# Performance work log

Hardware: AMD Instinct MI355X
Metric: run time of the kernel (lower is better)

The kernel has to match this reference:

```python
import jax, jax.numpy as jnp
import numpy as np

S = 1    # support_num
K = 20   # KNN neighbor count for conv layers
B, V = 4, 4096


def _normalize(x, axis):
    n = jnp.linalg.norm(x, axis=axis, keepdims=True)
    return x / jnp.maximum(n, 1e-12)


def _knn(v, k):
    # v: (b, n, 3) -> (b, n, k) indices of k nearest (excluding self)
    sq = jnp.sum(v * v, axis=-1)
    dist = sq[:, :, None] + sq[:, None, :] - 2.0 * jnp.einsum('bic,bjc->bij', v, v)
    return jax.lax.top_k(-dist, k + 1)[1][:, :, 1:]


def _gather(feat, idx):
    # feat (b,n,c), idx (b,n,k) -> (b,n,k,c)
    return feat[jnp.arange(feat.shape[0])[:, None, None], idx]


def _dir_norm(verts, idx):
    nb = _gather(verts, idx)                       # (b,v,k,3)
    return _normalize(nb - verts[:, :, None, :], -1)


def _conv_surface(idx, verts, directions, kernel_num):
    b, v, k = idx.shape
    nd = _dir_norm(verts, idx)
    sd = _normalize(directions, 0)                 # (3, S*kernel_num)
    theta = jax.nn.relu(jnp.einsum('bvkc,cm->bvkm', nd, sd))
    theta = theta.reshape(b, v, k, S, kernel_num)
    return jnp.sum(jnp.max(theta, axis=2), axis=2)  # (b,v,kernel_num)


def _conv_layer(idx, verts, fm, W, bias, directions, out_c):
    b, v, k = idx.shape
    nd = _dir_norm(verts, idx)
    sd = _normalize(directions, 0)                 # (3, S*out_c)
    theta = jax.nn.relu(jnp.einsum('bvkc,cm->bvkm', nd, sd))  # (b,v,k,S*out_c)
    fo = fm @ W + bias                             # (b,v,(S+1)*out_c)
    center = fo[:, :, :out_c]
    support = _gather(fo[:, :, out_c:], idx)       # (b,v,k,S*out_c)
    act = (theta * support).reshape(b, v, k, S, out_c)
    return center + jnp.sum(jnp.max(act, axis=2), axis=2)


def _pool(verts, fm, rate, nn, seed):
    b, v, _ = verts.shape
    idx = _knn(verts, nn)
    pooled = jnp.max(_gather(fm, idx), axis=2)
    sel = jax.random.permutation(jax.random.key(seed), v)[: v // rate]
    return verts[:, sel, :], pooled[:, sel, :]


def _ln(x, g, b):
    m = jnp.mean(x, -1, keepdims=True)
    var = jnp.mean(jnp.square(x - m), -1, keepdims=True)
    return (x - m) / jnp.sqrt(var + 1e-6) * g + b


def _mha(q, kv, Win, bin_, Wout, bout, h):
    E = q.shape[-1]
    hd = E // h
    wq, wk, wv = jnp.split(Win, 3, axis=0)
    bq, bk, bv = jnp.split(bin_, 3)

    def heads(x, w, bb_):
        y = x @ w.T + bb_
        return y.reshape(y.shape[0], y.shape[1], h, hd).transpose(0, 2, 1, 3)

    qh, kh, vh = heads(q, wq, bq), heads(kv, wk, bk), heads(kv, wv, bv)
    a = jax.nn.softmax(jnp.einsum('bhqd,bhkd->bhqk', qh, kh) / jnp.sqrt(jnp.float32(hd)), -1)
    o = jnp.einsum('bhqk,bhkd->bhqd', a, vh).transpose(0, 2, 1, 3).reshape(q.shape)
    return o @ Wout.T + bout


def _conv1x1(x, W, b):
    # x (B,C,N,1) -> (B,O,N,1)
    return jnp.einsum('bcnl,oc->bonl', x, W) + b[None, :, None, None]


def _bn_train(x, g, b):
    # BatchNorm2d in training mode (batch statistics), eps=1e-5
    m = jnp.mean(x, axis=(0, 2, 3), keepdims=True)
    v = jnp.var(x, axis=(0, 2, 3), keepdims=True)
    return (x - m) / jnp.sqrt(v + 1e-5) * g[None, :, None, None] + b[None, :, None, None]


def _forward(vertices, d0, g0, be0, w1, b1, dir1, g1, be1, w2, b2, dir2, g2, be2,
             w3, b3, dir3, g3, be3, token, a1_in_w, a1_in_b, a1_out_w, a1_out_b,
             ffn1_w, ffn1_b, bg, bb, ffn2_w, ffn2_b, a2_in_w, a2_in_b, a2_out_w,
             a2_out_b, w7, b7, dir7, g4, be4, c8_w, c8_b):
    b = vertices.shape[0]
    v0 = vertices[:, 0]                                 # (b, 4096, 3)
    idx0 = _knn(v0, K)
    fm0 = jax.nn.relu(_ln(_conv_surface(idx0, v0, d0, 32), g0, be0))
    fm1 = jax.nn.relu(_ln(_conv_layer(idx0, v0, fm0, w1, b1, dir1, 64), g1, be1))
    v1, fm1 = _pool(v0, fm1, 4, 4, 1)                   # (b,1024,3), (b,1024,64)
    idx1 = _knn(v1, K)
    fm_x = fm1
    fm2 = jax.nn.relu(_ln(_conv_layer(idx1, v1, fm1, w2, b2, dir2, 128), g2, be2))
    fm3 = jax.nn.relu(_ln(_conv_layer(idx1, v1, fm2, w3, b3, dir3, 256), g3, be3))
    _, fm3 = _pool(v1, fm3, 4, 4, 2)                    # (b,256,256)
    tok = jnp.tile(token, (b, 1, 1, 1))[:, :, :, 0].transpose(0, 2, 1)  # (b,1024,64)
    query = _mha(tok, fm_x, a1_in_w, a1_in_b, a1_out_w, a1_out_b, 4) + fm_x
    q2 = query.transpose(0, 2, 1)[:, :, :, None]        # (b,64,1024,1)
    q2 = _conv1x1(jax.nn.relu(_bn_train(_conv1x1(q2, ffn1_w, ffn1_b), bg, bb)), ffn2_w, ffn2_b)
    query = q2[:, :, :, 0].transpose(0, 2, 1)           # (b,1024,256)
    cross = _mha(query, fm3, a2_in_w, a2_in_b, a2_out_w, a2_out_b, 4) + query
    fmf = jax.nn.relu(_ln(_conv_layer(idx1, v1, cross, w7, b7, dir7, 1024), g4, be4))
    fmf = fmf.transpose(0, 2, 1)[:, :, :, None]         # (b,1024,1024,1)
    return _conv1x1(fmf, c8_w, c8_b)                    # (b,256,1024,1)


def setup_inputs():
    ks = iter(jax.random.split(jax.random.key(0), 64))

    def rn(shape, s=0.05):
        return jax.random.normal(next(ks), shape, dtype=jnp.float32) * s

    f32 = jnp.float32
    return dict(
        vertices=jax.random.normal(next(ks), (B, 1, V, 3), dtype=f32),
        d0=rn((3, S * 32)), g0=jnp.ones((32,), f32), be0=jnp.zeros((32,), f32),
        w1=rn((32, (S + 1) * 64)), b1=rn(((S + 1) * 64,)), dir1=rn((3, S * 64)),
        g1=jnp.ones((64,), f32), be1=jnp.zeros((64,), f32),
        w2=rn((64, (S + 1) * 128)), b2=rn(((S + 1) * 128,)), dir2=rn((3, S * 128)),
        g2=jnp.ones((128,), f32), be2=jnp.zeros((128,), f32),
        w3=rn((128, (S + 1) * 256)), b3=rn(((S + 1) * 256,)), dir3=rn((3, S * 256)),
        g3=jnp.ones((256,), f32), be3=jnp.zeros((256,), f32),
        token=rn((1, 64, 1024, 1), 1.0),
        a1_in_w=rn((192, 64)), a1_in_b=rn((192,)), a1_out_w=rn((64, 64)), a1_out_b=rn((64,)),
        ffn1_w=rn((256, 64)), ffn1_b=rn((256,)), bg=jnp.ones((256,), f32), bb=jnp.zeros((256,), f32),
        ffn2_w=rn((256, 256)), ffn2_b=rn((256,)),
        a2_in_w=rn((768, 256)), a2_in_b=rn((768,)), a2_out_w=rn((256, 256)), a2_out_b=rn((256,)),
        w7=rn((256, (S + 1) * 1024)), b7=rn(((S + 1) * 1024,)), dir7=rn((3, S * 1024)),
        g4=jnp.ones((1024,), f32), be4=jnp.zeros((1024,), f32),
        c8_w=rn((256, 1024)), c8_b=rn((256,)),
    )


def reference(vertices, d0, g0, be0, w1, b1, dir1, g1, be1, w2, b2, dir2, g2, be2,
              w3, b3, dir3, g3, be3, token, a1_in_w, a1_in_b, a1_out_w, a1_out_b,
              ffn1_w, ffn1_b, bg, bb, ffn2_w, ffn2_b, a2_in_w, a2_in_b, a2_out_w,
              a2_out_b, w7, b7, dir7, g4, be4, c8_w, c8_b):
    return _forward(vertices, d0, g0, be0, w1, b1, dir1, g1, be1, w2, b2, dir2, g2,
                    be2, w3, b3, dir3, g3, be3, token, a1_in_w, a1_in_b, a1_out_w,
                    a1_out_b, ffn1_w, ffn1_b, bg, bb, ffn2_w, ffn2_b, a2_in_w,
                    a2_in_b, a2_out_w, a2_out_b, w7, b7, dir7, g4, be4, c8_w, c8_b)
```

## Files before the change

kernel.cpp:

```cpp
#include <hip/hip_runtime.h>
#include <stdint.h>
#include <stddef.h>

#define FINF __builtin_inff()

__device__ inline void tf2x32(uint32_t k0, uint32_t k1, uint32_t x0, uint32_t x1,
                              uint32_t* o0, uint32_t* o1) {
  uint32_t ks2 = k0 ^ k1 ^ 0x1BD11BDAu;
  uint32_t v0 = x0 + k0, v1 = x1 + k1;
#define TFR(r) { v0 += v1; v1 = (v1 << (r)) | (v1 >> (32 - (r))); v1 ^= v0; }
  TFR(13) TFR(15) TFR(26) TFR(6)
  v0 += k1;  v1 += ks2 + 1u;
  TFR(17) TFR(29) TFR(16) TFR(24)
  v0 += ks2; v1 += k0 + 2u;
  TFR(13) TFR(15) TFR(26) TFR(6)
  v0 += k0;  v1 += k1 + 3u;
  TFR(17) TFR(29) TFR(16) TFR(24)
  v0 += k1;  v1 += ks2 + 4u;
  TFR(13) TFR(15) TFR(26) TFR(6)
  v0 += ks2; v1 += k0 + 5u;
#undef TFR
  *o0 = v0; *o1 = v1;
}

__global__ __launch_bounds__(1024) void perm_both_kernel(int* __restrict__ sel1,
                                                         int* __restrict__ sel2) {
  __shared__ unsigned long long keys[4096];
  __shared__ int vals[4096];
  __shared__ uint32_t kst[2];
  __shared__ uint32_t sk[2];
  uint32_t seed = (blockIdx.x == 0) ? 1u : 2u;
  int n       = (blockIdx.x == 0) ? 4096 : 1024;
  int rounds  = (blockIdx.x == 0) ? 2 : 1;
  int m       = (blockIdx.x == 0) ? 1024 : 256;
  int* out    = (blockIdx.x == 0) ? sel1 : sel2;
  int t = threadIdx.x;
  for (int i = t; i < n; i += 1024) vals[i] = i;
  if (t == 0) { kst[0] = 0u; kst[1] = seed; }
  __syncthreads();
  for (int r = 0; r < rounds; r++) {
    if (t == 0) {
      uint32_t a0, a1, b0, b1;
      tf2x32(kst[0], kst[1], 0u, 0u, &a0, &a1);
      tf2x32(kst[0], kst[1], 0u, 1u, &b0, &b1);
      kst[0] = a0; kst[1] = a1; sk[0] = b0; sk[1] = b1;
    }
    __syncthreads();
    uint32_t s0 = sk[0], s1 = sk[1];
    for (int i = t; i < n; i += 1024) {
      uint32_t y0, y1; tf2x32(s0, s1, 0u, (uint32_t)i, &y0, &y1);
      keys[i] = ((unsigned long long)(y0 ^ y1) << 32) | (unsigned)i;
    }
    __syncthreads();
    for (int kk = 2; kk <= n; kk <<= 1) {
      for (int j = kk >> 1; j > 0; j >>= 1) {
        for (int i = t; i < n; i += 1024) {
          int l = i ^ j;
          if (l > i) {
            unsigned long long ki = keys[i], kl = keys[l];
            bool up = ((i & kk) == 0);
            if (up ? (ki > kl) : (ki < kl)) {
              keys[i] = kl; keys[l] = ki;
              int v = vals[i]; vals[i] = vals[l]; vals[l] = v;
            }
          }
        }
        __syncthreads();
      }
    }
  }
  for (int i = t; i < m; i += 1024) out[i] = vals[i];
}

__device__ inline void wave_argmin2(float head_d, int head_i, float* Mo, int* wio) {
  float M = head_d;
#pragma unroll
  for (int off = 1; off < 64; off <<= 1) M = fminf(M, __shfl_xor(M, off));
  int cand = (head_d == M) ? head_i : 0x7fffffff;
#pragma unroll
  for (int off = 1; off < 64; off <<= 1) cand = min(cand, __shfl_xor(cand, off));
  *Mo = M; *wio = cand;
}

template <int CNT, int WAVES>
__global__ __launch_bounds__(64 * WAVES) void knn_lex_kernel(const float* __restrict__ verts,
                                                             int N,
                                                             int* __restrict__ idx20,
                                                             int* __restrict__ idx4) {
  int row = blockIdx.x; int b = row / N, i = row - b * N;
  int t = threadIdx.x; int w = t >> 6; int lane = t & 63;
  const float* vb = verts + (size_t)b * N * 3;
  float xi = vb[i * 3], yi = vb[i * 3 + 1], zi = vb[i * 3 + 2];
  float sqi = (xi * xi + yi * yi) + zi * zi;

  int base = w * (N / WAVES) + lane;
  float qd[CNT]; int qi[CNT];
#pragma unroll
  for (int m = 0; m < CNT; m++) {
    int j = base + m * 64;
    float xj = vb[j * 3], yj = vb[j * 3 + 1], zj = vb[j * 3 + 2];
    float sqj = (xj * xj + yj * yj) + zj * zj;
    float dot = (xi * xj + yi * yj) + zi * zj;
    qd[m] = sqi + sqj - 2.f * dot;
    qi[m] = j;
  }
#pragma unroll
  for (int k = 2; k <= CNT; k <<= 1)
#pragma unroll
    for (int j = k >> 1; j > 0; j >>= 1)
#pragma unroll
      for (int m = 0; m < CNT; m++) {
        int l = m ^ j;
        if (l > m) {
          bool up = ((m & k) == 0);
          bool sw = up ? (qd[m] > qd[l]) : (qd[m] < qd[l]);
          float td = sw ? qd[l] : qd[m]; qd[l] = sw ? qd[m] : qd[l]; qd[m] = td;
          int ti = sw ? qi[l] : qi[m]; qi[l] = sw ? qi[m] : qi[l]; qi[m] = ti;
        }
      }

  __shared__ float wd[WAVES][21];
  __shared__ int wi[WAVES][21];
  for (int r = 0; r < 21; r++) {
    float M; int widx;
    wave_argmin2(qd[0], qi[0], &M, &widx);
    if (lane == 0) { wd[w][r] = M; wi[w][r] = widx; }
    bool win = (qi[0] == widx);
#pragma unroll
    for (int m = 0; m < CNT - 1; m++) {
      qd[m] = win ? qd[m + 1] : qd[m];
      qi[m] = win ? qi[m + 1] : qi[m];
    }
    if (win) { qd[CNT - 1] = FINF; qi[CNT - 1] = 0x7fffffff; }
  }
  __syncthreads();
  if (lane < 21) {
    float d0 = wd[w][lane]; int i0 = wi[w][lane];
    int rank = lane;
#pragma unroll
    for (int w2 = 0; w2 < WAVES; w2++) {
      if (w2 == w) continue;
      for (int p = 0; p < 21; p++) {
        float ld = wd[w2][p]; int li = wi[w2][p];
        rank += (ld < d0 || (ld == d0 && li < i0)) ? 1 : 0;
      }
    }
    if (rank >= 1 && rank <= 20) idx20[(size_t)row * 20 + (rank - 1)] = i0;
    if (rank >= 1 && rank <= 4)  idx4[(size_t)row * 4 + (rank - 1)] = i0;
  }
}

template <int CNT>
__global__ __launch_bounds__(64) void knn_1w_lex_kernel(const float* __restrict__ verts, int N,
                                                        int* __restrict__ idx20,
                                                        int* __restrict__ idx4) {
  int row = blockIdx.x; int b = row / N, i = row - b * N;
  int lane = threadIdx.x;
  const float* vb = verts + (size_t)b * N * 3;
  float xi = vb[i * 3], yi = vb[i * 3 + 1], zi = vb[i * 3 + 2];
  float sqi = (xi * xi + yi * yi) + zi * zi;

  float qd[CNT]; int qi[CNT];
#pragma unroll
  for (int m = 0; m < CNT; m++) {
    int j = lane + m * 64;
    float xj = vb[j * 3], yj = vb[j * 3 + 1], zj = vb[j * 3 + 2];
    float sqj = (xj * xj + yj * yj) + zj * zj;
    float dot = (xi * xj + yi * yj) + zi * zj;
    qd[m] = sqi + sqj - 2.f * dot;
    qi[m] = j;
  }
#pragma unroll
  for (int k = 2; k <= CNT; k <<= 1)
#pragma unroll
    for (int j = k >> 1; j > 0; j >>= 1)
#pragma unroll
      for (int m = 0; m < CNT; m++) {
        int l = m ^ j;
        if (l > m) {
          bool up = ((m & k) == 0);
          bool sw = up ? (qd[m] > qd[l]) : (qd[m] < qd[l]);
          float td = sw ? qd[l] : qd[m]; qd[l] = sw ? qd[m] : qd[l]; qd[m] = td;
          int ti = sw ? qi[l] : qi[m]; qi[l] = sw ? qi[m] : qi[l]; qi[m] = ti;
        }
      }
  for (int r = 0; r < 21; r++) {
    float M; int widx;
    wave_argmin2(qd[0], qi[0], &M, &widx);
    if (lane == 0 && r >= 1) {
      idx20[(size_t)row * 20 + (r - 1)] = widx;
      if (r <= 4) idx4[(size_t)row * 4 + (r - 1)] = widx;
    }
    bool win = (qi[0] == widx);
#pragma unroll
    for (int m = 0; m < CNT - 1; m++) {
      qd[m] = win ? qd[m + 1] : qd[m];
      qi[m] = win ? qi[m + 1] : qi[m];
    }
    if (win) { qd[CNT - 1] = FINF; qi[CNT - 1] = 0x7fffffff; }
  }
}

__global__ void conv_surface_kernel(const float* __restrict__ verts,
                                    const int* __restrict__ idx20,
                                    const float* __restrict__ d0,
                                    const float* __restrict__ g, const float* __restrict__ be,
                                    float* __restrict__ out, int N) {
  int row = blockIdx.x; int b = row / N, i = row - b * N;
  int t = threadIdx.x;
  __shared__ float nd[20][3];
  const float* vb = verts + (size_t)b * N * 3;
  if (t < 20) {
    int j = idx20[(size_t)row * 20 + t];
    float dx = vb[j * 3] - vb[i * 3], dy = vb[j * 3 + 1] - vb[i * 3 + 1], dz = vb[j * 3 + 2] - vb[i * 3 + 2];
    float n2 = sqrtf(dx * dx + dy * dy + dz * dz); n2 = fmaxf(n2, 1e-12f);
    nd[t][0] = dx / n2; nd[t][1] = dy / n2; nd[t][2] = dz / n2;
  }
  __syncthreads();
  float x = 0.f;
  if (t < 32) {
    float a = d0[t], bb2 = d0[32 + t], c = d0[64 + t];
    float nrm = fmaxf(sqrtf(a * a + bb2 * bb2 + c * c), 1e-12f);
    a /= nrm; bb2 /= nrm; c /= nrm;
    float mx = -FINF;
    for (int kk = 0; kk < 20; kk++) {
      float th = fmaxf(nd[kk][0] * a + nd[kk][1] * bb2 + nd[kk][2] * c, 0.f);
      mx = fmaxf(mx, th);
    }
    x = mx;
  }
  float s = x;
  for (int off = 32; off; off >>= 1) s += __shfl_xor(s, off);
  float mean = s / 32.f;
  float dev = (t < 32) ? x - mean : 0.f;
  float s2 = dev * dev;
  for (int off = 32; off; off >>= 1) s2 += __shfl_xor(s2, off);
  float var = s2 / 32.f;
  if (t < 32) {
    float y = (x - mean) / sqrtf(var + 1e-6f) * g[t] + be[t];
    out[(size_t)row * 32 + t] = fmaxf(y, 0.f);
  }
}

__global__ void gemm_io_kernel(const float* __restrict__ x, const float* __restrict__ W,
                               const float* __restrict__ bias, float* __restrict__ y,
                               int R, int I, int O) {
  int rb = blockIdx.x * 8;
  int o = blockIdx.y * blockDim.x + threadIdx.x;
  __shared__ float xs[256][8];
  for (int u = 0; u < 8; u++)
    for (int i2 = threadIdx.x; i2 < I; i2 += blockDim.x) xs[i2][u] = x[(size_t)(rb + u) * I + i2];
  __syncthreads();
  float a[8] = {0, 0, 0, 0, 0, 0, 0, 0};
  for (int k2 = 0; k2 < I; k2++) {
    float wv = W[(size_t)k2 * O + o];
    float4 xa = *(const float4*)&xs[k2][0];
    float4 xb = *(const float4*)&xs[k2][4];
    a[0] += xa.x * wv; a[1] += xa.y * wv; a[2] += xa.z * wv; a[3] += xa.w * wv;
    a[4] += xb.x * wv; a[5] += xb.y * wv; a[6] += xb.z * wv; a[7] += xb.w * wv;
  }
  float bv = bias[o];
#pragma unroll
  for (int u = 0; u < 8; u++) y[(size_t)(rb + u) * O + o] = a[u] + bv;
}

template <int CPT>
__global__ void combine_kernel(const float* __restrict__ verts, const int* __restrict__ idx20,
                               const float* __restrict__ fo, const float* __restrict__ dirs,
                               const float* __restrict__ g, const float* __restrict__ be,
                               float* __restrict__ out, int N, int C) {
  int row = blockIdx.x; int b = row / N, i = row - b * N;
  int t = threadIdx.x, bs = blockDim.x;
  __shared__ float nd[20][3];
  __shared__ int nidx[20];
  __shared__ float red[8];
  const float* vb = verts + (size_t)b * N * 3;
  if (t < 20) {
    int j = idx20[(size_t)row * 20 + t];
    nidx[t] = j;
    float dx = vb[j * 3] - vb[i * 3], dy = vb[j * 3 + 1] - vb[i * 3 + 1], dz = vb[j * 3 + 2] - vb[i * 3 + 2];
    float n2 = fmaxf(sqrtf(dx * dx + dy * dy + dz * dz), 1e-12f);
    nd[t][0] = dx / n2; nd[t][1] = dy / n2; nd[t][2] = dz / n2;
  }
  __syncthreads();
  const float* fob = fo + (size_t)b * N * 2 * C;
  const float* forow = fob + (size_t)i * 2 * C;
  float da[CPT], db[CPT], dc[CPT], mx[CPT];
#pragma unroll
  for (int u = 0; u < CPT; u++) {
    int c = t + u * bs;
    float a = dirs[c], bb = dirs[C + c], cc = dirs[2 * C + c];
    float nrm = fmaxf(sqrtf(a * a + bb * bb + cc * cc), 1e-12f);
    da[u] = a / nrm; db[u] = bb / nrm; dc[u] = cc / nrm;
    mx[u] = -FINF;
  }
  for (int kk = 0; kk < 20; kk++) {
    float n0 = nd[kk][0], n1 = nd[kk][1], n2v = nd[kk][2];
    const float* sup = fob + (size_t)nidx[kk] * 2 * C + C + t;
#pragma unroll
    for (int u = 0; u < CPT; u++) {
      float th = fmaxf(n0 * da[u] + n1 * db[u] + n2v * dc[u], 0.f);
      mx[u] = fmaxf(mx[u], th * sup[u * bs]);
    }
  }
  float xv[CPT];
  float ssum = 0.f;
#pragma unroll
  for (int u = 0; u < CPT; u++) {
    int c = t + u * bs;
    float val = forow[c] + mx[u];
    xv[u] = val; ssum += val;
  }
  int nw = bs >> 6;
  for (int off = 32; off; off >>= 1) ssum += __shfl_down(ssum, off);
  if ((t & 63) == 0) red[t >> 6] = ssum;
  __syncthreads();
  if (t == 0) { float s = red[0]; for (int w = 1; w < nw; w++) s += red[w]; red[0] = s; }
  __syncthreads();
  float mean = red[0] / (float)C;
  __syncthreads();
  float s2 = 0.f;
#pragma unroll
  for (int u = 0; u < CPT; u++) { float d2 = xv[u] - mean; s2 += d2 * d2; }
  for (int off = 32; off; off >>= 1) s2 += __shfl_down(s2, off);
  if ((t & 63) == 0) red[t >> 6] = s2;
  __syncthreads();
  if (t == 0) { float s = red[0]; for (int w = 1; w < nw; w++) s += red[w]; red[0] = s; }
  __syncthreads();
  float inv = 1.0f / sqrtf(red[0] / (float)C + 1e-6f);
#pragma unroll
  for (int u = 0; u < CPT; u++) {
    int c = t + u * bs;
    float yv = (xv[u] - mean) * inv * g[c] + be[c];
    out[(size_t)row * C + c] = fmaxf(yv, 0.f);
  }
}

__global__ void pool_select_kernel(const float* __restrict__ fm, const int* __restrict__ idx4,
                                   const int* __restrict__ sel, const float* __restrict__ vin,
                                   float* __restrict__ vout, float* __restrict__ out,
                                   int N, int M, int C) {
  int row = blockIdx.x; int b = row / M, r = row - b * M;
  int s = sel[r];
  const int* id = idx4 + ((size_t)b * N + s) * 4;
  int i0 = id[0], i1 = id[1], i2 = id[2], i3 = id[3];
  const float* fb = fm + (size_t)b * N * C;
  for (int c = threadIdx.x; c < C; c += blockDim.x) {
    float m = fmaxf(fmaxf(fb[(size_t)i0 * C + c], fb[(size_t)i1 * C + c]),
                    fmaxf(fb[(size_t)i2 * C + c], fb[(size_t)i3 * C + c]));
    out[((size_t)b * M + r) * C + c] = m;
  }
  if (vout != nullptr && threadIdx.x < 3)
    vout[((size_t)b * M + r) * 3 + threadIdx.x] = vin[((size_t)b * N + s) * 3 + threadIdx.x];
}

__global__ void tok_kernel(const float* __restrict__ token, float* __restrict__ tok) {
  int id = blockIdx.x * 256 + threadIdx.x;
  int e = id & 63; int n = (id >> 6) & 1023;
  tok[id] = token[e * 1024 + n];
}

__global__ void linear_oi_kernel(const float* __restrict__ x, const float* __restrict__ W,
                                 const float* __restrict__ bias, const float* __restrict__ res,
                                 float* __restrict__ y, int R, int I, int O) {
  int rb = blockIdx.x * 8;
  int o = threadIdx.x;
  __shared__ float xs[8][256];
  for (int u = 0; u < 8; u++)
    for (int i2 = threadIdx.x; i2 < I; i2 += O) xs[u][i2] = x[(size_t)(rb + u) * I + i2];
  __syncthreads();
  float a[8] = {0, 0, 0, 0, 0, 0, 0, 0};
  const float* w = W + (size_t)o * I;
  for (int k2 = 0; k2 < I; k2++) {
    float wv = w[k2];
#pragma unroll
    for (int u = 0; u < 8; u++) a[u] += xs[u][k2] * wv;
  }
  float bv = bias[o];
#pragma unroll
  for (int u = 0; u < 8; u++) {
    float val = a[u] + bv;
    if (res) val += res[(size_t)(rb + u) * O + o];
    y[(size_t)(rb + u) * O + o] = val;
  }
}

template <int HD, int QPT, int KS>
__global__ __launch_bounds__(256) void attn_tiled(
    const float* __restrict__ q, const float* __restrict__ kk,
    const float* __restrict__ vv, float* __restrict__ o,
    int Lq, int Lk, int H, float scale) {
  constexpr int TK = 64;
  constexpr int QG = 256 / (2 * KS);
  constexpr int QPB = QG * QPT;
  constexpr int V4 = HD / 4;
  constexpr int STR = V4 + 1;
  constexpr int HH = HD / 2;
  constexpr int V4H = HH / 4;

  __shared__ float4 Ks[TK * STR];
  __shared__ float4 Vs[TK * STR];

  int t = threadIdx.x;
  int dh = t & 1;
  int ki = (t >> 1) & (KS - 1);
  int qg = t / (2 * KS);
  int nqt = Lq / QPB;
  int qt = blockIdx.x % nqt, bh = blockIdx.x / nqt;
  int h = bh % H, b = bh / H;
  int E = H * HD;
  int q0 = qt * QPB + qg * QPT;

  const float* qbase = q + ((size_t)b * Lq + q0) * E + h * HD + dh * HH;
  const float* kbase = kk + (size_t)b * Lk * E + h * HD;
  const float* vbase = vv + (size_t)b * Lk * E + h * HD;

  float qr[QPT][HH], O[QPT][HH], m[QPT], l[QPT];
#pragma unroll
  for (int r = 0; r < QPT; r++) {
    m[r] = -FINF; l[r] = 0.f;
#pragma unroll
    for (int d = 0; d < HH; d++) { qr[r][d] = qbase[(size_t)r * E + d]; O[r][d] = 0.f; }
  }

  for (int k0 = 0; k0 < Lk; k0 += TK) {
    __syncthreads();
    for (int e = t; e < TK * V4; e += 256) {
      int rr = e / V4, cc = e - rr * V4;
      Ks[rr * STR + cc] = *(const float4*)(kbase + (size_t)(k0 + rr) * E + cc * 4);
      Vs[rr * STR + cc] = *(const float4*)(vbase + (size_t)(k0 + rr) * E + cc * 4);
    }
    __syncthreads();
#pragma unroll 1
    for (int g = 0; g < TK / KS; g += 4) {
      float sc[QPT][4];
#pragma unroll
      for (int jj = 0; jj < 4; jj++) {
        int kl = (g + jj) * KS + ki;
        float sh[QPT];
#pragma unroll
        for (int r = 0; r < QPT; r++) sh[r] = 0.f;
        const float4* kr = &Ks[kl * STR + dh * V4H];
#pragma unroll
        for (int c = 0; c < V4H; c++) {
          float4 kv = kr[c];
#pragma unroll
          for (int r = 0; r < QPT; r++)
            sh[r] += qr[r][4 * c] * kv.x + qr[r][4 * c + 1] * kv.y
                   + qr[r][4 * c + 2] * kv.z + qr[r][4 * c + 3] * kv.w;
        }
#pragma unroll
        for (int r = 0; r < QPT; r++)
          sc[r][jj] = (sh[r] + __shfl_xor(sh[r], 1)) * scale;
      }
#pragma unroll
      for (int r = 0; r < QPT; r++) {
        float tm = fmaxf(fmaxf(sc[r][0], sc[r][1]), fmaxf(sc[r][2], sc[r][3]));
        float nm = fmaxf(m[r], tm);
        float a = __expf(m[r] - nm);
        m[r] = nm;
        float ls = l[r] * a;
#pragma unroll
        for (int d = 0; d < HH; d++) O[r][d] *= a;
#pragma unroll
        for (int jj = 0; jj < 4; jj++) { sc[r][jj] = __expf(sc[r][jj] - nm); ls += sc[r][jj]; }
        l[r] = ls;
      }
#pragma unroll
      for (int jj = 0; jj < 4; jj++) {
        int kl = (g + jj) * KS + ki;
        const float4* vr = &Vs[kl * STR + dh * V4H];
#pragma unroll
        for (int c = 0; c < V4H; c++) {
          float4 v4 = vr[c];
#pragma unroll
          for (int r = 0; r < QPT; r++) {
            O[r][4 * c]     += sc[r][jj] * v4.x;
            O[r][4 * c + 1] += sc[r][jj] * v4.y;
            O[r][4 * c + 2] += sc[r][jj] * v4.z;
            O[r][4 * c + 3] += sc[r][jj] * v4.w;
          }
        }
      }
    }
  }
#pragma unroll
  for (int r = 0; r < QPT; r++) {
    float M = m[r];
#pragma unroll
    for (int mask = 2; mask < 2 * KS; mask <<= 1) M = fmaxf(M, __shfl_xor(M, mask));
    float w = __expf(m[r] - M);
    float ll = l[r] * w;
#pragma unroll
    for (int mask = 2; mask < 2 * KS; mask <<= 1) ll += __shfl_xor(ll, mask);
    float inv = 1.f / ll;
#pragma unroll
    for (int d = 0; d < HH; d++) {
      float x = O[r][d] * w;
#pragma unroll
      for (int mask = 2; mask < 2 * KS; mask <<= 1) x += __shfl_xor(x, mask);
      O[r][d] = x * inv;
    }
  }
  if (ki == 0) {
    float* obase = o + ((size_t)b * Lq + q0) * E + h * HD + dh * HH;
#pragma unroll
    for (int r = 0; r < QPT; r++)
#pragma unroll
      for (int d = 0; d < HH; d++) obase[(size_t)r * E + d] = O[r][d];
  }
}

__global__ void bn_stats_kernel(const float* __restrict__ x, float* __restrict__ stats,
                                int R, int C) {
  int c = blockIdx.x; int t = threadIdx.x;
  __shared__ float red[8];
  float s = 0.f;
  for (int r = t; r < R; r += blockDim.x) s += x[(size_t)r * C + c];
  for (int off = 32; off; off >>= 1) s += __shfl_down(s, off);
  if ((t & 63) == 0) red[t >> 6] = s;
  __syncthreads();
  if (t == 0) { float a = red[0]; for (int w = 1; w < (int)(blockDim.x >> 6); w++) a += red[w]; red[0] = a; }
  __syncthreads();
  float mean = red[0] / (float)R;
  __syncthreads();
  float s2 = 0.f;
  for (int r = t; r < R; r += blockDim.x) { float d = x[(size_t)r * C + c] - mean; s2 += d * d; }
  for (int off = 32; off; off >>= 1) s2 += __shfl_down(s2, off);
  if ((t & 63) == 0) red[t >> 6] = s2;
  __syncthreads();
  if (t == 0) {
    float a = red[0]; for (int w = 1; w < (int)(blockDim.x >> 6); w++) a += red[w];
    stats[c] = mean; stats[C + c] = a / (float)R;
  }
}

__global__ void bn_apply_kernel(float* __restrict__ x, const float* __restrict__ stats,
                                const float* __restrict__ g, const float* __restrict__ b2,
                                int total, int C) {
  int id = blockIdx.x * blockDim.x + threadIdx.x;
  if (id >= total) return;
  int c = id % C;
  float y = (x[id] - stats[c]) / sqrtf(stats[C + c] + 1e-5f) * g[c] + b2[c];
  x[id] = fmaxf(y, 0.f);
}

__global__ void final_kernel(const float* __restrict__ fmf, const float* __restrict__ W,
                             const float* __restrict__ bias, float* __restrict__ out) {
  int nb = blockIdx.x * 8;
  int o = threadIdx.x;
  __shared__ float xs[1024][8];
  for (int u = 0; u < 8; u++)
    for (int c = threadIdx.x; c < 1024; c += 256) xs[c][u] = fmf[(size_t)(nb + u) * 1024 + c];
  __syncthreads();
  float acc[8] = {0, 0, 0, 0, 0, 0, 0, 0};
  const float* w = W + (size_t)o * 1024;
  for (int c = 0; c < 1024; c++) {
    float wv = w[c];
    float4 xa = *(const float4*)&xs[c][0];
    float4 xb = *(const float4*)&xs[c][4];
    acc[0] += xa.x * wv; acc[1] += xa.y * wv; acc[2] += xa.z * wv; acc[3] += xa.w * wv;
    acc[4] += xb.x * wv; acc[5] += xb.y * wv; acc[6] += xb.z * wv; acc[7] += xb.w * wv;
  }
  float bv = bias[o];
#pragma unroll
  for (int u = 0; u < 8; u++) {
    int r = nb + u; int b = r >> 10; int n = r & 1023;
    out[((size_t)(b * 256 + o) << 10) + n] = acc[u] + bv;
  }
}

extern "C" void kernel_launch(void* const* d_in, const int* in_sizes, int n_in,
                              void* d_out, int out_size, void* d_ws, size_t ws_size,
                              hipStream_t stream) {
  (void)in_sizes; (void)n_in; (void)out_size;
  const float* vertices = (const float*)d_in[0];
  const float* d0       = (const float*)d_in[1];
  const float* g0       = (const float*)d_in[2];
  const float* be0      = (const float*)d_in[3];
  const float* w1       = (const float*)d_in[4];
  const float* b1       = (const float*)d_in[5];
  const float* dir1     = (const float*)d_in[6];
  const float* g1       = (const float*)d_in[7];
  const float* be1      = (const float*)d_in[8];
  const float* w2       = (const float*)d_in[9];
  const float* b2       = (const float*)d_in[10];
  const float* dir2     = (const float*)d_in[11];
  const float* g2       = (const float*)d_in[12];
  const float* be2      = (const float*)d_in[13];
  const float* w3       = (const float*)d_in[14];
  const float* b3       = (const float*)d_in[15];
  const float* dir3     = (const float*)d_in[16];
  const float* g3       = (const float*)d_in[17];
  const float* be3      = (const float*)d_in[18];
  const float* token    = (const float*)d_in[19];
  const float* a1_in_w  = (const float*)d_in[20];
  const float* a1_in_b  = (const float*)d_in[21];
  const float* a1_out_w = (const float*)d_in[22];
  const float* a1_out_b = (const float*)d_in[23];
  const float* ffn1_w   = (const float*)d_in[24];
  const float* ffn1_b   = (const float*)d_in[25];
  const float* bg       = (const float*)d_in[26];
  const float* bbp      = (const float*)d_in[27];
  const float* ffn2_w   = (const float*)d_in[28];
  const float* ffn2_b   = (const float*)d_in[29];
  const float* a2_in_w  = (const float*)d_in[30];
  const float* a2_in_b  = (const float*)d_in[31];
  const float* a2_out_w = (const float*)d_in[32];
  const float* a2_out_b = (const float*)d_in[33];
  const float* w7       = (const float*)d_in[34];
  const float* b7       = (const float*)d_in[35];
  const float* dir7     = (const float*)d_in[36];
  const float* g4       = (const float*)d_in[37];
  const float* be4      = (const float*)d_in[38];
  const float* c8_w     = (const float*)d_in[39];
  const float* c8_b     = (const float*)d_in[40];
  float* out = (float*)d_out;
  float* ws = (float*)d_ws;

  if (ws_size < 78568448u) return;

  float* FO     = ws + 0;
  float* S1     = ws + 8388608;
  float* S2     = ws + 12582912;
  float* S3     = ws + 13631488;
  float* QUERY2 = ws + 14680064;
  float* CROSS  = ws + 15728640;
  float* FM1P   = ws + 16777216;
  float* FM3P   = FM1P + 262144;
  float* TOK    = FM3P + 262144;
  float* Q1     = TOK + 262144;
  float* K1     = Q1 + 262144;
  float* VA1    = K1 + 262144;
  float* ATT1   = VA1 + 262144;
  float* K2     = ATT1 + 262144;
  float* V2     = K2 + 262144;
  float* V1     = V2 + 262144;
  float* BNST   = V1 + 12288;
  int* IDX20_0  = (int*)(BNST + 512);
  int* IDX4_0   = IDX20_0 + 327680;
  int* IDX20_1  = IDX4_0 + 65536;
  int* IDX4_1   = IDX20_1 + 81920;
  int* SEL1     = IDX4_1 + 16384;
  int* SEL2     = SEL1 + 1024;

  perm_both_kernel<<<2, 1024, 0, stream>>>(SEL1, SEL2);

  knn_lex_kernel<32, 2><<<4 * 4096, 128, 0, stream>>>(vertices, 4096, IDX20_0, IDX4_0);
  conv_surface_kernel<<<4 * 4096, 64, 0, stream>>>(vertices, IDX20_0, d0, g0, be0, S2, 4096);
  gemm_io_kernel<<<dim3(2048, 1), 128, 0, stream>>>(S2, w1, b1, FO, 16384, 32, 128);
  combine_kernel<1><<<16384, 64, 0, stream>>>(vertices, IDX20_0, FO, dir1, g1, be1, S1, 4096, 64);
  pool_select_kernel<<<4096, 64, 0, stream>>>(S1, IDX4_0, SEL1, vertices, V1, FM1P, 4096, 1024, 64);

  knn_1w_lex_kernel<16><<<4 * 1024, 64, 0, stream>>>(V1, 1024, IDX20_1, IDX4_1);
  gemm_io_kernel<<<dim3(512, 1), 256, 0, stream>>>(FM1P, w2, b2, FO, 4096, 64, 256);
  combine_kernel<1><<<4096, 128, 0, stream>>>(V1, IDX20_1, FO, dir2, g2, be2, S2, 1024, 128);
  gemm_io_kernel<<<dim3(512, 2), 256, 0, stream>>>(S2, w3, b3, FO, 4096, 128, 512);
  combine_kernel<1><<<4096, 256, 0, stream>>>(V1, IDX20_1, FO, dir3, g3, be3, S3, 1024, 256);
  pool_select_kernel<<<1024, 256, 0, stream>>>(S3, IDX4_1, SEL2, nullptr, nullptr, FM3P, 1024, 256, 256);

  tok_kernel<<<1024, 256, 0, stream>>>(token, TOK);
  linear_oi_kernel<<<512, 64, 0, stream>>>(TOK, a1_in_w, a1_in_b, nullptr, Q1, 4096, 64, 64);
  linear_oi_kernel<<<512, 64, 0, stream>>>(FM1P, a1_in_w + 64 * 64, a1_in_b + 64, nullptr, K1, 4096, 64, 64);
  linear_oi_kernel<<<512, 64, 0, stream>>>(FM1P, a1_in_w + 128 * 64, a1_in_b + 128, nullptr, VA1, 4096, 64, 64);
  attn_tiled<16, 4, 8><<<256, 256, 0, stream>>>(Q1, K1, VA1, ATT1, 1024, 1024, 4, 0.25f);
  linear_oi_kernel<<<512, 64, 0, stream>>>(ATT1, a1_out_w, a1_out_b, FM1P, S3, 4096, 64, 64);

  linear_oi_kernel<<<512, 256, 0, stream>>>(S3, ffn1_w, ffn1_b, nullptr, S2, 4096, 64, 256);
  bn_stats_kernel<<<256, 256, 0, stream>>>(S2, BNST, 4096, 256);
  bn_apply_kernel<<<4096, 256, 0, stream>>>(S2, BNST, bg, bbp, 4096 * 256, 256);
  linear_oi_kernel<<<512, 256, 0, stream>>>(S2, ffn2_w, ffn2_b, nullptr, QUERY2, 4096, 256, 256);

  linear_oi_kernel<<<512, 256, 0, stream>>>(QUERY2, a2_in_w, a2_in_b, nullptr, S3, 4096, 256, 256);
  linear_oi_kernel<<<128, 256, 0, stream>>>(FM3P, a2_in_w + 256 * 256, a2_in_b + 256, nullptr, K2, 1024, 256, 256);
  linear_oi_kernel<<<128, 256, 0, stream>>>(FM3P, a2_in_w + 512 * 256, a2_in_b + 512, nullptr, V2, 1024, 256, 256);
  attn_tiled<64, 2, 8><<<512, 256, 0, stream>>>(S3, K2, V2, S1, 1024, 256, 4, 0.125f);
  linear_oi_kernel<<<512, 256, 0, stream>>>(S1, a2_out_w, a2_out_b, QUERY2, CROSS, 4096, 256, 256);

  gemm_io_kernel<<<dim3(512, 8), 256, 0, stream>>>(CROSS, w7, b7, FO, 4096, 256, 2048);
  combine_kernel<4><<<4096, 256, 0, stream>>>(V1, IDX20_1, FO, dir7, g4, be4, S1, 1024, 1024);
  final_kernel<<<512, 256, 0, stream>>>(S1, c8_w, c8_b, out);
}
```

Baseline: 1.006 ms.

## Replace single-block bitonic permutation sort with parallel rank-by-counting kernels

Moves the random-permutation generation off a two-block bitonic sort in shared memory and onto multiple small kernels. One kernel generates threefry sort keys, the other computes each element's rank by counting smaller keys across many blocks, then scatters it. The sequential sort chain on one CU goes away in exchange for six launches and O(n^2) comparisons. Scratch keys live in the IDX20_0 buffer, which is overwritten later by the first KNN kernel.

After: 1.249 ms. +24.1%, slower.

```diff
diff --git a/kernel.cpp b/kernel.cpp
--- a/kernel.cpp
+++ b/kernel.cpp
@@ -23,53 +23,42 @@
   *o0 = v0; *o1 = v1;
 }
 
-__global__ __launch_bounds__(1024) void perm_both_kernel(int* __restrict__ sel1,
-                                                         int* __restrict__ sel2) {
-  __shared__ unsigned long long keys[4096];
-  __shared__ int vals[4096];
-  __shared__ uint32_t kst[2];
-  __shared__ uint32_t sk[2];
-  uint32_t seed = (blockIdx.x == 0) ? 1u : 2u;
-  int n       = (blockIdx.x == 0) ? 4096 : 1024;
-  int rounds  = (blockIdx.x == 0) ? 2 : 1;
-  int m       = (blockIdx.x == 0) ? 1024 : 256;
-  int* out    = (blockIdx.x == 0) ? sel1 : sel2;
+__device__ inline void perm_subkey(uint32_t seed, int round, uint32_t* s0, uint32_t* s1) {
+  uint32_t k0 = 0u, k1 = seed;
+  for (int r = 0; r < round; r++) {
+    uint32_t a0, a1; tf2x32(k0, k1, 0u, 0u, &a0, &a1);
+    k0 = a0; k1 = a1;
+  }
+  tf2x32(k0, k1, 0u, 1u, s0, s1);
+}
+
+__global__ __launch_bounds__(256) void perm_keys_kernel(uint32_t seed, int round, int n,
+                                                        unsigned long long* __restrict__ keys) {
+  uint32_t s0, s1; perm_subkey(seed, round, &s0, &s1);
+  int i = blockIdx.x * 256 + threadIdx.x;
+  if (i < n) {
+    uint32_t y0, y1; tf2x32(s0, s1, 0u, (uint32_t)i, &y0, &y1);
+    keys[i] = ((unsigned long long)(y0 ^ y1) << 32) | (unsigned)i;
+  }
+}
+
+__global__ __launch_bounds__(256) void perm_rank_kernel(const unsigned long long* __restrict__ keys,
+                                                        const int* __restrict__ vin,
+                                                        int* __restrict__ vout, int n, int m) {
+  __shared__ int part[256];
   int t = threadIdx.x;
-  for (int i = t; i < n; i += 1024) vals[i] = i;
-  if (t == 0) { kst[0] = 0u; kst[1] = seed; }
-  __syncthreads();
-  for (int r = 0; r < rounds; r++) {
-    if (t == 0) {
-      uint32_t a0, a1, b0, b1;
-      tf2x32(kst[0], kst[1], 0u, 0u, &a0, &a1);
-      tf2x32(kst[0], kst[1], 0u, 1u, &b0, &b1);
-      kst[0] = a0; kst[1] = a1; sk[0] = b0; sk[1] = b1;
-    }
-    __syncthreads();
-    uint32_t s0 = sk[0], s1 = sk[1];
-    for (int i = t; i < n; i += 1024) {
-      uint32_t y0, y1; tf2x32(s0, s1, 0u, (uint32_t)i, &y0, &y1);
-      keys[i] = ((unsigned long long)(y0 ^ y1) << 32) | (unsigned)i;
-    }
-    __syncthreads();
-    for (int kk = 2; kk <= n; kk <<= 1) {
-      for (int j = kk >> 1; j > 0; j >>= 1) {
-        for (int i = t; i < n; i += 1024) {
-          int l = i ^ j;
-          if (l > i) {
-            unsigned long long ki = keys[i], kl = keys[l];
-            bool up = ((i & kk) == 0);
-            if (up ? (ki > kl) : (ki < kl)) {
-              keys[i] = kl; keys[l] = ki;
-              int v = vals[i]; vals[i] = vals[l]; vals[l] = v;
-            }
-          }
-        }
-        __syncthreads();
-      }
-    }
-  }
-  for (int i = t; i < m; i += 1024) out[i] = vals[i];
+  int r = blockIdx.x * 128 + (t & 127);
+  int half = t >> 7;
+  unsigned long long ki = keys[r];
+  int cnt = 0;
+  int j0 = half * (n >> 1), j1 = j0 + (n >> 1);
+  for (int j = j0; j < j1; j++) cnt += (keys[j] < ki) ? 1 : 0;
+  part[t] = cnt;
+  __syncthreads();
+  if (t < 128) {
+    int rank = part[t] + part[t + 128];
+    if (rank < m) vout[rank] = vin ? vin[r] : r;
+  }
 }
 
 __device__ inline void wave_argmin2(float head_d, int head_i, float* Mo, int* wio) {
@@ -643,8 +632,15 @@
   int* IDX4_1   = IDX20_1 + 81920;
   int* SEL1     = IDX4_1 + 16384;
   int* SEL2     = SEL1 + 1024;
-
-  perm_both_kernel<<<2, 1024, 0, stream>>>(SEL1, SEL2);
+  unsigned long long* PK = (unsigned long long*)IDX20_0;
+  int* PT1 = IDX20_0 + 8192;
+
+  perm_keys_kernel<<<16, 256, 0, stream>>>(1u, 0, 4096, PK);
+  perm_rank_kernel<<<32, 256, 0, stream>>>(PK, nullptr, PT1, 4096, 4096);
+  perm_keys_kernel<<<16, 256, 0, stream>>>(1u, 1, 4096, PK);
+  perm_rank_kernel<<<32, 256, 0, stream>>>(PK, PT1, SEL1, 4096, 1024);
+  perm_keys_kernel<<<4, 256, 0, stream>>>(2u, 0, 1024, PK);
+  perm_rank_kernel<<<8, 256, 0, stream>>>(PK, nullptr, SEL2, 1024, 256);
 
   knn_lex_kernel<32, 2><<<4 * 4096, 128, 0, stream>>>(vertices, 4096, IDX20_0, IDX4_0);
   conv_surface_kernel<<<4 * 4096, 64, 0, stream>>>(vertices, IDX20_0, d0, g0, be0, S2, 4096);
```
